# Optimization experiments

Measured on AMD Instinct MI355X. Metric: run time of the kernel, lower is better.

## Reference

```python
import jax, jax.numpy as jnp
import numpy as np

N, B, D_IN, HID = 1024, 8, 256, 256
L, SH, LH, GH = 2, 2, 4, 2
H = SH + LH + GH
DH = HID // H
EPS = 1e-5


def _sinusoidal_pe(n, d):
    pos = np.arange(n, dtype=np.float32)[:, None]
    i = np.arange(d, dtype=np.float32)[None, :]
    angle = pos / np.power(10000.0, (2.0 * np.floor(i / 2.0)) / d)
    pe = np.where((np.arange(d) % 2) == 0, np.sin(angle), np.cos(angle))
    return jnp.asarray(pe, jnp.float32)  # (n, d)


def _ln(x, g, b):
    mu = x.mean(-1, keepdims=True)
    var = ((x - mu) ** 2).mean(-1, keepdims=True)
    return (x - mu) * jax.lax.rsqrt(var + EPS) * g + b


def setup_inputs() -> dict:
    key = jax.random.key(0)
    ks = jax.random.split(key, 16)
    s = 0.02
    inp = {
        "nodes": jax.random.normal(ks[0], (N, B, D_IN), jnp.float32),
        "dist": jax.random.randint(ks[1], (B, N, N), 0, 6, jnp.int32),
        "W_in": jax.random.normal(ks[2], (D_IN, HID), jnp.float32) * s,
        "b_in": jnp.zeros((HID,), jnp.float32),
        "ln_in_g": jnp.ones((HID,), jnp.float32),
        "ln_in_b": jnp.zeros((HID,), jnp.float32),
        "Wqkv": jax.random.normal(ks[3], (L, HID, 3 * HID), jnp.float32) * s,
        "bqkv": jnp.zeros((L, 3 * HID), jnp.float32),
        "Wo": jax.random.normal(ks[4], (L, HID, HID), jnp.float32) * s,
        "bo": jnp.zeros((L, HID), jnp.float32),
        "ln1_g": jnp.ones((L, HID), jnp.float32),
        "ln1_b": jnp.zeros((L, HID), jnp.float32),
        "W1": jax.random.normal(ks[5], (L, HID, 2 * HID), jnp.float32) * s,
        "b1": jnp.zeros((L, 2 * HID), jnp.float32),
        "W2": jax.random.normal(ks[6], (L, 2 * HID, HID), jnp.float32) * s,
        "b2": jnp.zeros((L, HID), jnp.float32),
        "ln2_g": jnp.ones((L, HID), jnp.float32),
        "ln2_b": jnp.zeros((L, HID), jnp.float32),
        "bn_g": jnp.ones((HID,), jnp.float32),
        "bn_b": jnp.zeros((HID,), jnp.float32),
    }
    return inp


def reference(nodes, dist, W_in, b_in, ln_in_g, ln_in_b, Wqkv, bqkv, Wo, bo,
              ln1_g, ln1_b, W1, b1, W2, b2, ln2_g, ln2_b, bn_g, bn_b):
    # positional embedding (sinusoidal, added) + dense + LayerNorm; dropout=eval (identity)
    x = nodes + _sinusoidal_pe(N, D_IN)[:, None, :]          # (N,B,D_IN)
    x = _ln(x @ W_in + b_in, ln_in_g, ln_in_b)               # (N,B,HID)

    # dist_to_mask: per-head-group allowed patterns; True in torch mask = disallowed
    short = (dist == 1)[:, None]                             # (B,1,N,N)
    longm = (dist >= 1)[:, None]
    allowed = jnp.concatenate([
        jnp.broadcast_to(short, (B, SH, N, N)),
        jnp.broadcast_to(longm, (B, LH, N, N)),
        jnp.ones((B, GH, N, N), bool),
    ], axis=1)                                               # (B,H,N,N)
    bias = jnp.where(allowed, 0.0, -jnp.inf).astype(x.dtype)

    scale = 1.0 / np.sqrt(DH)
    for l in range(L):
        qkv = x @ Wqkv[l] + bqkv[l]                          # (N,B,3*HID)
        q, k, v = jnp.split(qkv, 3, axis=-1)
        def heads(t):  # (N,B,HID) -> (B,H,N,DH)
            return t.reshape(N, B, H, DH).transpose(1, 2, 0, 3)
        q, k, v = heads(q), heads(k), heads(v)
        s = jnp.einsum('bhnd,bhmd->bhnm', q, k) * scale + bias
        a = jax.nn.softmax(s, axis=-1)
        o = jnp.einsum('bhnm,bhmd->bhnd', a, v)              # (B,H,N,DH)
        o = o.transpose(2, 0, 1, 3).reshape(N, B, HID)
        x = _ln(x + o @ Wo[l] + bo[l], ln1_g[l], ln1_b[l])   # post-norm
        f = jax.nn.relu(x @ W1[l] + b1[l]) @ W2[l] + b2[l]
        x = _ln(x + f, ln2_g[l], ln2_b[l])

    y = x[0]                                                 # (B,HID) first position
    mu = y.mean(0)
    var = ((y - mu) ** 2).mean(0)
    return (y - mu) * jax.lax.rsqrt(var + EPS) * bn_g + bn_b
```

## Files before the change

### kernel.cpp

```cpp
#include <hip/hip_runtime.h>
#include <math.h>

constexpr int Nn = 1024, Bb = 8, HIDc = 256, Hh = 8, DHc = 32;
constexpr int TSTR = 520;

typedef __bf16 bf16x8 __attribute__((ext_vector_type(8)));
typedef __bf16 bf16x4 __attribute__((ext_vector_type(4)));
typedef float  f32x4  __attribute__((ext_vector_type(4)));

struct WCvtArgs {
    const float* src[9];
    int K[9], M[9], dstOff[9], tiles[9];
};

__global__ __launch_bounds__(256)
void prep_k(WCvtArgs a, __bf16* __restrict__ Wt,
            const int* __restrict__ dist, unsigned char* __restrict__ mp,
            const float* __restrict__ nodes, __bf16* __restrict__ xinb)
{
    __shared__ float ts[32][33];
    const int tid = threadIdx.x;
    if (blockIdx.x < 1088) {
        int bid = blockIdx.x, i = 0;
        while (bid >= a.tiles[i]) { bid -= a.tiles[i]; ++i; }
        const int K = a.K[i], M = a.M[i];
        const int tilesM = M >> 5;
        const int m0 = (bid % tilesM) << 5, k0 = (bid / tilesM) << 5;
        const float* src = a.src[i];
        __bf16* dst = Wt + a.dstOff[i];
        const int tx = tid & 31, ty = tid >> 5;
        #pragma unroll
        for (int j = 0; j < 4; ++j)
            ts[ty + 8 * j][tx] = src[(size_t)(k0 + ty + 8 * j) * M + m0 + tx];
        __syncthreads();
        #pragma unroll
        for (int j = 0; j < 4; ++j)
            dst[(size_t)(m0 + ty + 8 * j) * K + k0 + tx] = (__bf16)ts[tx][ty + 8 * j];
    } else if (blockIdx.x < 3136) {
        const int idx = (blockIdx.x - 1088) * 256 + tid;
        const int quad = idx & 3, c = (idx >> 2) & 15, q = (idx >> 6) & 1023, b = idx >> 16;
        const int* dp = dist + ((((size_t)b << 10) + q) << 10) + c * 64 + quad * 4;
        uchar4 out;
        unsigned char* po = &out.x;
        #pragma unroll
        for (int t = 0; t < 4; ++t) {
            const int4 v = *(const int4*)(dp + t * 16);
            unsigned int code = 0;
            const int dd[4] = {v.x, v.y, v.z, v.w};
            #pragma unroll
            for (int r = 0; r < 4; ++r)
                code |= ((dd[r] == 1 ? 1u : 0u) | (dd[r] >= 1 ? 2u : 0u)) << (2 * r);
            po[t] = (unsigned char)code;
        }
        *(uchar4*)(mp + ((((size_t)b << 10) + q) << 8) + (c << 4) + (quad << 2)) = out;
    } else {
        const int idx = (blockIdx.x - 3136) * 256 + tid;
        const int token = idx >> 7, k2 = (idx & 127) * 2;
        const int b = token >> 10, n = token & 1023;
        const float e = (float)k2 * (1.0f / 256.0f);
        const float freq = exp2f(-13.287712379549449f * e);
        const float ang = (float)n * freq;
        const float2 nd = *(const float2*)(nodes + ((size_t)(n * 8 + b)) * 256 + k2);
        __bf16* p = xinb + (size_t)token * 256 + k2;
        p[0] = (__bf16)(nd.x + sinf(ang));
        p[1] = (__bf16)(nd.y + cosf(ang));
    }
}

template<int KK, int NJ>
__device__ __forceinline__ void gemmT(const __bf16* __restrict__ wrow,
                                      const __bf16* __restrict__ x0,
                                      const __bf16* __restrict__ x1,
                                      f32x4 acc[4][2])
{
    constexpr int NKC = KK / 32;
    bf16x8 wA[4][4];
    #pragma unroll
    for (int p = 0; p < 4; ++p)
        #pragma unroll
        for (int t = 0; t < 4; ++t)
            wA[p][t] = *(const bf16x8*)(wrow + (size_t)(t * 16) * KK + p * 32);
    #pragma unroll
    for (int t = 0; t < 4; ++t) {
        acc[t][0] = (f32x4){0.f, 0.f, 0.f, 0.f};
        if (NJ == 2) acc[t][1] = (f32x4){0.f, 0.f, 0.f, 0.f};
    }
    #pragma unroll
    for (int kc = 0; kc < NKC; ++kc) {
        const bf16x8 b0 = *(const bf16x8*)(x0 + kc * 32);
        bf16x8 b1;
        if (NJ == 2) b1 = *(const bf16x8*)(x1 + kc * 32);
        const int cur = kc & 3;
        #pragma unroll
        for (int t = 0; t < 4; ++t) {
            acc[t][0] = __builtin_amdgcn_mfma_f32_16x16x32_bf16(wA[cur][t], b0, acc[t][0], 0, 0, 0);
            if (NJ == 2)
                acc[t][1] = __builtin_amdgcn_mfma_f32_16x16x32_bf16(wA[cur][t], b1, acc[t][1], 0, 0, 0);
        }
        if (kc + 4 < NKC)
            #pragma unroll
            for (int t = 0; t < 4; ++t)
                wA[cur][t] = *(const bf16x8*)(wrow + (size_t)(t * 16) * KK + (kc + 4) * 32);
    }
}

template<bool RESID, bool FFN, bool QKV, bool N0ROWS, bool XGATE, bool BNOUT, int NJ>
__global__ __launch_bounds__(256)
void layer_k(const __bf16* __restrict__ Ain, const float* __restrict__ xres,
             const __bf16* __restrict__ w0, const float* __restrict__ b0,
             const float* __restrict__ g1, const float* __restrict__ be1,
             const __bf16* __restrict__ w1, const float* __restrict__ b1_,
             const __bf16* __restrict__ w2, const float* __restrict__ b2_,
             const float* __restrict__ g2, const float* __restrict__ be2,
             const __bf16* __restrict__ wq, const float* __restrict__ bq, int qfull,
             const float* __restrict__ bng, const float* __restrict__ bnb,
             float* __restrict__ xout,
             __bf16* __restrict__ qb, __bf16* __restrict__ kb, __bf16* __restrict__ vtb)
{
    __shared__ __bf16 trans[32][TSTR];
    __shared__ float red[4][32][2];

    const int tid = threadIdx.x;
    const int lane = tid & 63;
    const int cq = tid >> 6;
    const int col = lane & 15, quad = lane >> 4;
    const int row0 = blockIdx.x * (NJ * 16);
    const int mb = cq * 64;

    #pragma unroll
    for (int i = 0; i < 2; ++i) {
        const int v = i * 256 + tid;
        const int rw = v >> 4, cc = (v & 15) * 16;
        const int rg = N0ROWS ? ((rw & 7) << 10) : (row0 + rw);
        *(bf16x8*)&trans[rw][cc]     = *(const bf16x8*)(Ain + (size_t)rg * 256 + cc);
        *(bf16x8*)&trans[rw][cc + 8] = *(const bf16x8*)(Ain + (size_t)rg * 256 + cc + 8);
    }
    __syncthreads();

    const __bf16* x0 = &trans[col][quad * 8];
    const __bf16* x1 = &trans[16 + col][quad * 8];
    int tg[2];
    #pragma unroll
    for (int j = 0; j < NJ; ++j)
        tg[j] = N0ROWS ? ((j * 16 + col) & 7) << 10 : (row0 + j * 16 + col);

    f32x4 acc[4][2];
    gemmT<256, NJ>(w0 + (size_t)(mb + col) * 256 + quad * 8, x0, x1, acc);

    float val[2][4][4];
    {
        float4 bb4[4], gm4[4], bt4[4];
        #pragma unroll
        for (int t = 0; t < 4; ++t) {
            const int cb = mb + t * 16 + quad * 4;
            bb4[t] = *(const float4*)&b0[cb];
            gm4[t] = *(const float4*)&g1[cb];
            bt4[t] = *(const float4*)&be1[cb];
        }
        #pragma unroll
        for (int j = 0; j < NJ; ++j) {
            float s1 = 0.f, s2 = 0.f;
            #pragma unroll
            for (int t = 0; t < 4; ++t) {
                float4 xr4 = {0.f, 0.f, 0.f, 0.f};
                if (RESID) xr4 = *(const float4*)&xres[(size_t)tg[j] * 256 + mb + t * 16 + quad * 4];
                const float* bbp = (const float*)&bb4[t];
                const float* xrp = (const float*)&xr4;
                #pragma unroll
                for (int r = 0; r < 4; ++r) {
                    float v = acc[t][j][r] + bbp[r] + xrp[r];
                    val[j][t][r] = v; s1 += v; s2 += v * v;
                }
            }
            s1 += __shfl_xor(s1, 16); s1 += __shfl_xor(s1, 32);
            s2 += __shfl_xor(s2, 16); s2 += __shfl_xor(s2, 32);
            if (quad == 0) { red[cq][j * 16 + col][0] = s1; red[cq][j * 16 + col][1] = s2; }
        }
        __syncthreads();
        #pragma unroll
        for (int j = 0; j < NJ; ++j) {
            const int tk = j * 16 + col;
            const float s1 = red[0][tk][0] + red[1][tk][0] + red[2][tk][0] + red[3][tk][0];
            const float s2 = red[0][tk][1] + red[1][tk][1] + red[2][tk][1] + red[3][tk][1];
            const float mu = s1 * (1.0f / 256.0f);
            const float rv = rsqrtf(s2 * (1.0f / 256.0f) - mu * mu + 1e-5f);
            #pragma unroll
            for (int t = 0; t < 4; ++t) {
                const float* gmp = (const float*)&gm4[t];
                const float* btp = (const float*)&bt4[t];
                bf16x4 o4; float4 of;
                #pragma unroll
                for (int r = 0; r < 4; ++r) {
                    const float o = (val[j][t][r] - mu) * rv * gmp[r] + btp[r];
                    val[j][t][r] = o;
                    o4[r] = (__bf16)o;
                    ((float*)&of)[r] = o;
                }
                *(bf16x4*)&trans[tk][mb + t * 16 + quad * 4] = o4;
                if (!FFN)
                    *(float4*)&xout[(size_t)tg[j] * 256 + mb + t * 16 + quad * 4] = of;
            }
        }
        __syncthreads();
    }

    if (FFN) {
        bf16x4 h1p[2][2][4];
        #pragma unroll
        for (int mh = 0; mh < 2; ++mh) {
            f32x4 a1[4][2];
            gemmT<256, NJ>(w1 + (size_t)(mh * 256 + mb + col) * 256 + quad * 8, x0, x1, a1);
            #pragma unroll
            for (int t = 0; t < 4; ++t) {
                const float4 bh4 = *(const float4*)&b1_[mh * 256 + mb + t * 16 + quad * 4];
                const float* bhp = (const float*)&bh4;
                #pragma unroll
                for (int j = 0; j < NJ; ++j)
                    #pragma unroll
                    for (int r = 0; r < 4; ++r)
                        h1p[mh][j][t][r] = (__bf16)fmaxf(a1[t][j][r] + bhp[r], 0.f);
            }
        }
        __syncthreads();
        #pragma unroll
        for (int mh = 0; mh < 2; ++mh)
            #pragma unroll
            for (int j = 0; j < NJ; ++j)
                #pragma unroll
                for (int t = 0; t < 4; ++t)
                    *(bf16x4*)&trans[j * 16 + col][mh * 256 + mb + t * 16 + quad * 4] = h1p[mh][j][t];
        __syncthreads();

        f32x4 a2[4][2];
        gemmT<512, NJ>(w2 + (size_t)(mb + col) * 512 + quad * 8, x0, x1, a2);

        float4 bb4[4], gm4[4], bt4[4];
        #pragma unroll
        for (int t = 0; t < 4; ++t) {
            const int cb = mb + t * 16 + quad * 4;
            bb4[t] = *(const float4*)&b2_[cb];
            gm4[t] = *(const float4*)&g2[cb];
            bt4[t] = *(const float4*)&be2[cb];
        }
        #pragma unroll
        for (int j = 0; j < NJ; ++j) {
            float s1 = 0.f, s2 = 0.f;
            #pragma unroll
            for (int t = 0; t < 4; ++t) {
                const float* bbp = (const float*)&bb4[t];
                #pragma unroll
                for (int r = 0; r < 4; ++r) {
                    const float v = a2[t][j][r] + bbp[r] + val[j][t][r];
                    val[j][t][r] = v; s1 += v; s2 += v * v;
                }
            }
            s1 += __shfl_xor(s1, 16); s1 += __shfl_xor(s1, 32);
            s2 += __shfl_xor(s2, 16); s2 += __shfl_xor(s2, 32);
            if (quad == 0) { red[cq][j * 16 + col][0] = s1; red[cq][j * 16 + col][1] = s2; }
        }
        __syncthreads();
        #pragma unroll
        for (int j = 0; j < NJ; ++j) {
            const int tk = j * 16 + col;
            const float s1 = red[0][tk][0] + red[1][tk][0] + red[2][tk][0] + red[3][tk][0];
            const float s2 = red[0][tk][1] + red[1][tk][1] + red[2][tk][1] + red[3][tk][1];
            const float mu = s1 * (1.0f / 256.0f);
            const float rv = rsqrtf(s2 * (1.0f / 256.0f) - mu * mu + 1e-5f);
            #pragma unroll
            for (int t = 0; t < 4; ++t) {
                const float* gmp = (const float*)&gm4[t];
                const float* btp = (const float*)&bt4[t];
                bf16x4 o4; float4 of;
                #pragma unroll
                for (int r = 0; r < 4; ++r) {
                    const float o = (val[j][t][r] - mu) * rv * gmp[r] + btp[r];
                    val[j][t][r] = o;
                    o4[r] = (__bf16)o;
                    ((float*)&of)[r] = o;
                }
                if (QKV) *(bf16x4*)&trans[tk][mb + t * 16 + quad * 4] = o4;
                if (!BNOUT) {
                    const bool wr = XGATE ? ((tg[j] & 1023) == 0) : true;
                    if (wr) *(float4*)&xout[(size_t)tg[j] * 256 + mb + t * 16 + quad * 4] = of;
                }
            }
        }
        if (BNOUT) {
            #pragma unroll
            for (int t = 0; t < 4; ++t) {
                const int cb = mb + t * 16 + quad * 4;
                const float4 g4 = *(const float4*)&bng[cb];
                const float4 bB = *(const float4*)&bnb[cb];
                float4 of;
                #pragma unroll
                for (int r = 0; r < 4; ++r) {
                    float s1 = val[0][t][r], s2 = val[0][t][r] * val[0][t][r];
                    s1 += __shfl_xor(s1, 1); s2 += __shfl_xor(s2, 1);
                    s1 += __shfl_xor(s1, 2); s2 += __shfl_xor(s2, 2);
                    s1 += __shfl_xor(s1, 4); s2 += __shfl_xor(s2, 4);
                    s1 += __shfl_xor(s1, 8); s2 += __shfl_xor(s2, 8);
                    const float mu = s1 * (1.0f / 16.0f);
                    const float rv = rsqrtf(s2 * (1.0f / 16.0f) - mu * mu + 1e-5f);
                    ((float*)&of)[r] = (val[0][t][r] - mu) * rv * ((const float*)&g4)[r]
                                       + ((const float*)&bB)[r];
                }
                if (col < 8)
                    *(float4*)&xout[(size_t)col * 256 + cb] = of;
            }
        }
        __syncthreads();
    }

    if (QKV) {
        const int b_ = N0ROWS ? 0 : (row0 >> 10);
        const bool qneed = qfull || ((row0 & 1023) < 128);
        for (int cg = 0; cg < 3; ++cg) {
            if (cg == 0 && !qneed) continue;
            f32x4 aq[4][2];
            gemmT<256, NJ>(wq + (size_t)(cg * 256 + mb + col) * 256 + quad * 8, x0, x1, aq);
            const float qs = (cg == 0) ? 0.25505402616305625f : 1.0f;
            #pragma unroll
            for (int t = 0; t < 4; ++t) {
                const int cc = mb + t * 16;
                const int h = cc >> 5;
                const int dhb = (cc & 31) + quad * 4;
                const float4 bq4 = *(const float4*)&bq[cg * 256 + cc + quad * 4];
                const float* bqp = (const float*)&bq4;
                #pragma unroll
                for (int j = 0; j < NJ; ++j) {
                    const int n = tg[j] & 1023;
                    if (cg == 2) {
                        #pragma unroll
                        for (int r = 0; r < 4; ++r)
                            vtb[((size_t)(b_ * 8 + h) * 32 + dhb + r) * 1024 + n] =
                                (__bf16)(aq[t][j][r] + bqp[r]);
                    } else {
                        bf16x4 p;
                        #pragma unroll
                        for (int r = 0; r < 4; ++r)
                            p[r] = (__bf16)((aq[t][j][r] + bqp[r]) * qs);
                        __bf16* dst = (cg == 0) ? qb : kb;
                        *(bf16x4*)&dst[((size_t)(b_ * 8 + h) * 1024 + n) * 32 + dhb] = p;
                    }
                }
            }
        }
    }
}

__global__ __launch_bounds__(256)
void attn_mfma(const __bf16* __restrict__ Qb, const __bf16* __restrict__ Kb,
               const __bf16* __restrict__ Vt, const unsigned char* __restrict__ MP,
               __bf16* __restrict__ O)
{
    __shared__ __bf16 pbuf[2][4][2][16][72];
    const int tid = threadIdx.x;
    const int lane = tid & 63;
    const int wv = tid >> 6;
    const int col = lane & 15;
    const int quad = lane >> 4;
    const int xr = blockIdx.x;
    const int bh = ((xr & 7) << 3) | (xr >> 3);
    const int b = bh >> 3, h = bh & 7;
    const int qbase = blockIdx.y * 128 + wv * 32;
    const int hsel = (h < 2) ? 0 : 1;
    const bool masked = (h < 6);

    bf16x8 qf[2];
    #pragma unroll
    for (int j = 0; j < 2; ++j)
        qf[j] = *(const bf16x8*)(Qb + ((size_t)bh * Nn + qbase + j * 16 + col) * DHc + quad * 8);

    bf16x8 onesf;
    {
        const __bf16 one = (__bf16)1.0f, zero = (__bf16)0.0f;
        #pragma unroll
        for (int j = 0; j < 8; ++j) onesf[j] = (col == 0) ? one : zero;
    }

    f32x4 O0[2], O1[2], OL[2];
    #pragma unroll
    for (int j = 0; j < 2; ++j) {
        O0[j] = (f32x4){0.f, 0.f, 0.f, 0.f};
        O1[j] = (f32x4){0.f, 0.f, 0.f, 0.f};
        OL[j] = (f32x4){0.f, 0.f, 0.f, 0.f};
    }
    const f32x4 zf = {0.f, 0.f, 0.f, 0.f};
    const __bf16* kbase = Kb + (size_t)bh * Nn * DHc;

    bf16x8 kf[4];
    #pragma unroll
    for (int t = 0; t < 4; ++t)
        kf[t] = *(const bf16x8*)(kbase + (size_t)(t * 16 + col) * DHc + quad * 8);

    for (int c = 0; c < 16; ++c) {
        bf16x8 kn[4];
        if (c < 15)
            #pragma unroll
            for (int t = 0; t < 4; ++t)
                kn[t] = *(const bf16x8*)(kbase + (size_t)((c + 1) * 64 + t * 16 + col) * DHc + quad * 8);
        uchar4 mk[2];
        if (masked)
            #pragma unroll
            for (int j = 0; j < 2; ++j)
                mk[j] = *(const uchar4*)(MP + ((((size_t)b << 10) + qbase + j * 16 + col) << 8)
                                            + (c << 4) + (quad << 2));
        #pragma unroll
        for (int j = 0; j < 2; ++j) {
            f32x4 S[4];
            #pragma unroll
            for (int t = 0; t < 4; ++t)
                S[t] = __builtin_amdgcn_mfma_f32_16x16x32_bf16(kf[t], qf[j], zf, 0, 0, 0);
            if (masked) {
                const unsigned char mb2[4] = {mk[j].x, mk[j].y, mk[j].z, mk[j].w};
                #pragma unroll
                for (int t = 0; t < 4; ++t)
                    #pragma unroll
                    for (int r = 0; r < 4; ++r)
                        if (!((mb2[t] >> (2 * r + hsel)) & 1)) S[t][r] = -INFINITY;
            }
            #pragma unroll
            for (int t = 0; t < 4; ++t) {
                bf16x4 p4;
                #pragma unroll
                for (int r = 0; r < 4; ++r)
                    p4[r] = (__bf16)__builtin_amdgcn_exp2f(S[t][r]);
                *(bf16x4*)(&pbuf[c & 1][wv][j][col][t * 16 + quad * 4]) = p4;
            }
        }
        const __bf16* vp = Vt + (size_t)bh * DHc * Nn + c * 64 + quad * 8;
        #pragma unroll
        for (int kh = 0; kh < 2; ++kh) {
            const bf16x8 v0 = *(const bf16x8*)(vp + (size_t)col * Nn + kh * 32);
            const bf16x8 v1 = *(const bf16x8*)(vp + (size_t)(col + 16) * Nn + kh * 32);
            #pragma unroll
            for (int j = 0; j < 2; ++j) {
                const bf16x8 pf = *(const bf16x8*)(&pbuf[c & 1][wv][j][col][kh * 32 + quad * 8]);
                O0[j] = __builtin_amdgcn_mfma_f32_16x16x32_bf16(pf, v0, O0[j], 0, 0, 0);
                O1[j] = __builtin_amdgcn_mfma_f32_16x16x32_bf16(pf, v1, O1[j], 0, 0, 0);
                OL[j] = __builtin_amdgcn_mfma_f32_16x16x32_bf16(pf, onesf, OL[j], 0, 0, 0);
            }
        }
        if (c < 15)
            #pragma unroll
            for (int t = 0; t < 4; ++t) kf[t] = kn[t];
    }
    #pragma unroll
    for (int j = 0; j < 2; ++j)
        #pragma unroll
        for (int r = 0; r < 4; ++r) {
            const float Lr = __shfl(OL[j][r], lane & 48);
            const float inv = 1.0f / Lr;
            const int q = qbase + j * 16 + quad * 4 + r;
            __bf16* op = O + ((size_t)(b * 1024 + q)) * 256 + h * 32 + col;
            op[0]  = (__bf16)(O0[j][r] * inv);
            op[16] = (__bf16)(O1[j][r] * inv);
        }
}

extern "C" void kernel_launch(void* const* d_in, const int* in_sizes, int n_in,
                              void* d_out, int out_size, void* d_ws, size_t ws_size,
                              hipStream_t stream)
{
    const float* nodes   = (const float*)d_in[0];
    const int*   dist    = (const int*)  d_in[1];
    const float* W_in    = (const float*)d_in[2];
    const float* b_in    = (const float*)d_in[3];
    const float* ln_in_g = (const float*)d_in[4];
    const float* ln_in_b = (const float*)d_in[5];
    const float* Wqkv    = (const float*)d_in[6];
    const float* bqkv    = (const float*)d_in[7];
    const float* Wo      = (const float*)d_in[8];
    const float* bo      = (const float*)d_in[9];
    const float* ln1_g   = (const float*)d_in[10];
    const float* ln1_b   = (const float*)d_in[11];
    const float* W1      = (const float*)d_in[12];
    const float* b1      = (const float*)d_in[13];
    const float* W2      = (const float*)d_in[14];
    const float* b2      = (const float*)d_in[15];
    const float* ln2_g   = (const float*)d_in[16];
    const float* ln2_b   = (const float*)d_in[17];
    const float* bn_g    = (const float*)d_in[18];
    const float* bn_b    = (const float*)d_in[19];

    char* ws = (char*)d_ws;
    float*  x   = (float*)(ws);
    unsigned char* mp = (unsigned char*)(ws + 8388608);
    __bf16* wt  = (__bf16*)(ws + 10485760);
    __bf16* qb  = (__bf16*)(ws + 12845056);
    __bf16* kb  = (__bf16*)(ws + 17039360);
    __bf16* vtb = (__bf16*)(ws + 21233664);
    __bf16* ob  = (__bf16*)(ws + 25427968);
    __bf16* xinb = ob;

    WCvtArgs wa;
    wa.src[0] = W_in;           wa.K[0] = 256; wa.M[0] = 256; wa.dstOff[0] = 0;
    wa.src[1] = Wqkv;           wa.K[1] = 256; wa.M[1] = 768; wa.dstOff[1] = 65536;
    wa.src[2] = Wqkv + 196608;  wa.K[2] = 256; wa.M[2] = 768; wa.dstOff[2] = 262144;
    wa.src[3] = Wo;             wa.K[3] = 256; wa.M[3] = 256; wa.dstOff[3] = 458752;
    wa.src[4] = Wo + 65536;     wa.K[4] = 256; wa.M[4] = 256; wa.dstOff[4] = 524288;
    wa.src[5] = W1;             wa.K[5] = 256; wa.M[5] = 512; wa.dstOff[5] = 589824;
    wa.src[6] = W1 + 131072;    wa.K[6] = 256; wa.M[6] = 512; wa.dstOff[6] = 720896;
    wa.src[7] = W2;             wa.K[7] = 512; wa.M[7] = 256; wa.dstOff[7] = 851968;
    wa.src[8] = W2 + 131072;    wa.K[8] = 512; wa.M[8] = 256; wa.dstOff[8] = 983040;
    for (int i = 0; i < 9; ++i) wa.tiles[i] = (wa.K[i] >> 5) * (wa.M[i] >> 5);

    prep_k<<<7232, 256, 0, stream>>>(wa, wt, dist, mp, nodes, xinb);

    layer_k<false, false, true, false, false, false, 2><<<256, 256, 0, stream>>>(
        xinb, nullptr, wt, b_in, ln_in_g, ln_in_b,
        nullptr, nullptr, nullptr, nullptr, nullptr, nullptr,
        wt + 65536, bqkv, 1, nullptr, nullptr, x, qb, kb, vtb);

    attn_mfma<<<dim3(64, 8), 256, 0, stream>>>(qb, kb, vtb, mp, ob);

    layer_k<true, true, true, false, true, false, 2><<<256, 256, 0, stream>>>(
        ob, x, wt + 458752, bo, ln1_g, ln1_b,
        wt + 589824, b1, wt + 851968, b2, ln2_g, ln2_b,
        wt + 262144, bqkv + 768, 0, nullptr, nullptr, x, qb, kb, vtb);

    attn_mfma<<<dim3(64, 1), 256, 0, stream>>>(qb, kb, vtb, mp, ob);

    layer_k<true, true, false, true, true, true, 1><<<1, 256, 0, stream>>>(
        ob, x, wt + 524288, bo + 256, ln1_g + 256, ln1_b + 256,
        wt + 720896, b1 + 512, wt + 983040, b2 + 256, ln2_g + 256, ln2_b + 256,
        nullptr, nullptr, 0, bn_g, bn_b, (float*)d_out, nullptr, nullptr, nullptr);
}
```

Baseline: 267.3 us.

## Split layer kernel output columns across 8 waves instead of 4

The fused layer kernel now launches 512 threads per block, with each of 8 waves computing 32 output columns (one head) instead of 64. The GEMM helper is rewritten to hold 2 column tiles with 8-deep K-chunk weight prefetch, and the LayerNorm reductions sum over 8 wave partials. This is meant to double wave-level parallelism and hide weight-load latency in the latency-bound per-row-block GEMMs. In exchange it adds more barrier participants and a larger reduction buffer, and each wave reuses its activation operands over fewer tiles.

```diff
diff --git a/kernel.cpp b/kernel.cpp
--- a/kernel.cpp
+++ b/kernel.cpp
@@ -68,44 +68,69 @@
 }
 
 template<int KK, int NJ>
-__device__ __forceinline__ void gemmT(const __bf16* __restrict__ wrow,
+__device__ __forceinline__ void gemmW(const __bf16* __restrict__ wrow,
                                       const __bf16* __restrict__ x0,
                                       const __bf16* __restrict__ x1,
-                                      f32x4 acc[4][2])
+                                      f32x4 acc[2][2])
 {
     constexpr int NKC = KK / 32;
-    bf16x8 wA[4][4];
-    #pragma unroll
-    for (int p = 0; p < 4; ++p)
-        #pragma unroll
-        for (int t = 0; t < 4; ++t)
-            wA[p][t] = *(const bf16x8*)(wrow + (size_t)(t * 16) * KK + p * 32);
-    #pragma unroll
-    for (int t = 0; t < 4; ++t) {
+    bf16x8 wA[2][8];
+    #pragma unroll
+    for (int kc = 0; kc < (NKC > 8 ? 8 : NKC); ++kc)
+        #pragma unroll
+        for (int t = 0; t < 2; ++t)
+            wA[t][kc] = *(const bf16x8*)(wrow + (size_t)(t * 16) * KK + kc * 32);
+    #pragma unroll
+    for (int t = 0; t < 2; ++t) {
         acc[t][0] = (f32x4){0.f, 0.f, 0.f, 0.f};
         if (NJ == 2) acc[t][1] = (f32x4){0.f, 0.f, 0.f, 0.f};
     }
-    #pragma unroll
-    for (int kc = 0; kc < NKC; ++kc) {
-        const bf16x8 b0 = *(const bf16x8*)(x0 + kc * 32);
-        bf16x8 b1;
-        if (NJ == 2) b1 = *(const bf16x8*)(x1 + kc * 32);
-        const int cur = kc & 3;
-        #pragma unroll
-        for (int t = 0; t < 4; ++t) {
-            acc[t][0] = __builtin_amdgcn_mfma_f32_16x16x32_bf16(wA[cur][t], b0, acc[t][0], 0, 0, 0);
-            if (NJ == 2)
-                acc[t][1] = __builtin_amdgcn_mfma_f32_16x16x32_bf16(wA[cur][t], b1, acc[t][1], 0, 0, 0);
-        }
-        if (kc + 4 < NKC)
-            #pragma unroll
-            for (int t = 0; t < 4; ++t)
-                wA[cur][t] = *(const bf16x8*)(wrow + (size_t)(t * 16) * KK + (kc + 4) * 32);
+    if constexpr (NKC <= 8) {
+        #pragma unroll
+        for (int kc = 0; kc < NKC; ++kc) {
+            const bf16x8 b0 = *(const bf16x8*)(x0 + kc * 32);
+            bf16x8 b1;
+            if (NJ == 2) b1 = *(const bf16x8*)(x1 + kc * 32);
+            #pragma unroll
+            for (int t = 0; t < 2; ++t) {
+                acc[t][0] = __builtin_amdgcn_mfma_f32_16x16x32_bf16(wA[t][kc], b0, acc[t][0], 0, 0, 0);
+                if (NJ == 2)
+                    acc[t][1] = __builtin_amdgcn_mfma_f32_16x16x32_bf16(wA[t][kc], b1, acc[t][1], 0, 0, 0);
+            }
+        }
+    } else {
+        #pragma unroll
+        for (int kc = 0; kc < 8; ++kc) {
+            const bf16x8 b0 = *(const bf16x8*)(x0 + kc * 32);
+            bf16x8 b1;
+            if (NJ == 2) b1 = *(const bf16x8*)(x1 + kc * 32);
+            #pragma unroll
+            for (int t = 0; t < 2; ++t) {
+                acc[t][0] = __builtin_amdgcn_mfma_f32_16x16x32_bf16(wA[t][kc], b0, acc[t][0], 0, 0, 0);
+                if (NJ == 2)
+                    acc[t][1] = __builtin_amdgcn_mfma_f32_16x16x32_bf16(wA[t][kc], b1, acc[t][1], 0, 0, 0);
+            }
+            #pragma unroll
+            for (int t = 0; t < 2; ++t)
+                wA[t][kc] = *(const bf16x8*)(wrow + (size_t)(t * 16) * KK + (kc + 8) * 32);
+        }
+        #pragma unroll
+        for (int kc = 8; kc < 16; ++kc) {
+            const bf16x8 b0 = *(const bf16x8*)(x0 + kc * 32);
+            bf16x8 b1;
+            if (NJ == 2) b1 = *(const bf16x8*)(x1 + kc * 32);
+            #pragma unroll
+            for (int t = 0; t < 2; ++t) {
+                acc[t][0] = __builtin_amdgcn_mfma_f32_16x16x32_bf16(wA[t][kc - 8], b0, acc[t][0], 0, 0, 0);
+                if (NJ == 2)
+                    acc[t][1] = __builtin_amdgcn_mfma_f32_16x16x32_bf16(wA[t][kc - 8], b1, acc[t][1], 0, 0, 0);
+            }
+        }
     }
 }
 
 template<bool RESID, bool FFN, bool QKV, bool N0ROWS, bool XGATE, bool BNOUT, int NJ>
-__global__ __launch_bounds__(256)
+__global__ __launch_bounds__(512)
 void layer_k(const __bf16* __restrict__ Ain, const float* __restrict__ xres,
              const __bf16* __restrict__ w0, const float* __restrict__ b0,
              const float* __restrict__ g1, const float* __restrict__ be1,
@@ -118,22 +143,21 @@
              __bf16* __restrict__ qb, __bf16* __restrict__ kb, __bf16* __restrict__ vtb)
 {
     __shared__ __bf16 trans[32][TSTR];
-    __shared__ float red[4][32][2];
+    __shared__ float red[8][32][2];
 
     const int tid = threadIdx.x;
     const int lane = tid & 63;
-    const int cq = tid >> 6;
+    const int wv = tid >> 6;
     const int col = lane & 15, quad = lane >> 4;
     const int row0 = blockIdx.x * (NJ * 16);
-    const int mb = cq * 64;
-
-    #pragma unroll
-    for (int i = 0; i < 2; ++i) {
-        const int v = i * 256 + tid;
-        const int rw = v >> 4, cc = (v & 15) * 16;
+    const int ms = wv * 32;
+
+    #pragma unroll
+    for (int i = 0; i < NJ; ++i) {
+        const int v = i * 512 + tid;
+        const int rw = v >> 5, cc = (v & 31) * 8;
         const int rg = N0ROWS ? ((rw & 7) << 10) : (row0 + rw);
-        *(bf16x8*)&trans[rw][cc]     = *(const bf16x8*)(Ain + (size_t)rg * 256 + cc);
-        *(bf16x8*)&trans[rw][cc + 8] = *(const bf16x8*)(Ain + (size_t)rg * 256 + cc + 8);
+        *(bf16x8*)&trans[rw][cc] = *(const bf16x8*)(Ain + (size_t)rg * 256 + cc);
     }
     __syncthreads();
 
@@ -144,15 +168,15 @@
     for (int j = 0; j < NJ; ++j)
         tg[j] = N0ROWS ? ((j * 16 + col) & 7) << 10 : (row0 + j * 16 + col);
 
-    f32x4 acc[4][2];
-    gemmT<256, NJ>(w0 + (size_t)(mb + col) * 256 + quad * 8, x0, x1, acc);
-
-    float val[2][4][4];
+    f32x4 acc[2][2];
+    gemmW<256, NJ>(w0 + (size_t)(ms + col) * 256 + quad * 8, x0, x1, acc);
+
+    float val[2][2][4];
     {
-        float4 bb4[4], gm4[4], bt4[4];
-        #pragma unroll
-        for (int t = 0; t < 4; ++t) {
-            const int cb = mb + t * 16 + quad * 4;
+        float4 bb4[2], gm4[2], bt4[2];
+        #pragma unroll
+        for (int t = 0; t < 2; ++t) {
+            const int cb = ms + t * 16 + quad * 4;
             bb4[t] = *(const float4*)&b0[cb];
             gm4[t] = *(const float4*)&g1[cb];
             bt4[t] = *(const float4*)&be1[cb];
@@ -161,9 +185,9 @@
         for (int j = 0; j < NJ; ++j) {
             float s1 = 0.f, s2 = 0.f;
             #pragma unroll
-            for (int t = 0; t < 4; ++t) {
+            for (int t = 0; t < 2; ++t) {
                 float4 xr4 = {0.f, 0.f, 0.f, 0.f};
-                if (RESID) xr4 = *(const float4*)&xres[(size_t)tg[j] * 256 + mb + t * 16 + quad * 4];
+                if (RESID) xr4 = *(const float4*)&xres[(size_t)tg[j] * 256 + ms + t * 16 + quad * 4];
                 const float* bbp = (const float*)&bb4[t];
                 const float* xrp = (const float*)&xr4;
                 #pragma unroll
@@ -174,18 +198,19 @@
             }
             s1 += __shfl_xor(s1, 16); s1 += __shfl_xor(s1, 32);
             s2 += __shfl_xor(s2, 16); s2 += __shfl_xor(s2, 32);
-            if (quad == 0) { red[cq][j * 16 + col][0] = s1; red[cq][j * 16 + col][1] = s2; }
+            if (quad == 0) { red[wv][j * 16 + col][0] = s1; red[wv][j * 16 + col][1] = s2; }
         }
         __syncthreads();
         #pragma unroll
         for (int j = 0; j < NJ; ++j) {
             const int tk = j * 16 + col;
-            const float s1 = red[0][tk][0] + red[1][tk][0] + red[2][tk][0] + red[3][tk][0];
-            const float s2 = red[0][tk][1] + red[1][tk][1] + red[2][tk][1] + red[3][tk][1];
+            float s1 = 0.f, s2 = 0.f;
+            #pragma unroll
+            for (int w = 0; w < 8; ++w) { s1 += red[w][tk][0]; s2 += red[w][tk][1]; }
             const float mu = s1 * (1.0f / 256.0f);
             const float rv = rsqrtf(s2 * (1.0f / 256.0f) - mu * mu + 1e-5f);
             #pragma unroll
-            for (int t = 0; t < 4; ++t) {
+            for (int t = 0; t < 2; ++t) {
                 const float* gmp = (const float*)&gm4[t];
                 const float* btp = (const float*)&bt4[t];
                 bf16x4 o4; float4 of;
@@ -196,23 +221,23 @@
                     o4[r] = (__bf16)o;
                     ((float*)&of)[r] = o;
                 }
-                *(bf16x4*)&trans[tk][mb + t * 16 + quad * 4] = o4;
+                *(bf16x4*)&trans[tk][ms + t * 16 + quad * 4] = o4;
                 if (!FFN)
-                    *(float4*)&xout[(size_t)tg[j] * 256 + mb + t * 16 + quad * 4] = of;
+                    *(float4*)&xout[(size_t)tg[j] * 256 + ms + t * 16 + quad * 4] = of;
             }
         }
         __syncthreads();
     }
 
     if (FFN) {
-        bf16x4 h1p[2][2][4];
+        bf16x4 h1p[2][2][2];
         #pragma unroll
         for (int mh = 0; mh < 2; ++mh) {
-            f32x4 a1[4][2];
-            gemmT<256, NJ>(w1 + (size_t)(mh * 256 + mb + col) * 256 + quad * 8, x0, x1, a1);
-            #pragma unroll
-            for (int t = 0; t < 4; ++t) {
-                const float4 bh4 = *(const float4*)&b1_[mh * 256 + mb + t * 16 + quad * 4];
+            f32x4 a1[2][2];
+            gemmW<256, NJ>(w1 + (size_t)(mh * 256 + ms + col) * 256 + quad * 8, x0, x1, a1);
+            #pragma unroll
+            for (int t = 0; t < 2; ++t) {
+                const float4 bh4 = *(const float4*)&b1_[mh * 256 + ms + t * 16 + quad * 4];
                 const float* bhp = (const float*)&bh4;
                 #pragma unroll
                 for (int j = 0; j < NJ; ++j)
@@ -227,17 +252,17 @@
             #pragma unroll
             for (int j = 0; j < NJ; ++j)
                 #pragma unroll
-                for (int t = 0; t < 4; ++t)
-                    *(bf16x4*)&trans[j * 16 + col][mh * 256 + mb + t * 16 + quad * 4] = h1p[mh][j][t];
-        __syncthreads();
-
-        f32x4 a2[4][2];
-        gemmT<512, NJ>(w2 + (size_t)(mb + col) * 512 + quad * 8, x0, x1, a2);
-
-        float4 bb4[4], gm4[4], bt4[4];
-        #pragma unroll
-        for (int t = 0; t < 4; ++t) {
-            const int cb = mb + t * 16 + quad * 4;
+                for (int t = 0; t < 2; ++t)
+                    *(bf16x4*)&trans[j * 16 + col][mh * 256 + ms + t * 16 + quad * 4] = h1p[mh][j][t];
+        __syncthreads();
+
+        f32x4 a2[2][2];
+        gemmW<512, NJ>(w2 + (size_t)(ms + col) * 512 + quad * 8, x0, x1, a2);
+
+        float4 bb4[2], gm4[2], bt4[2];
+        #pragma unroll
+        for (int t = 0; t < 2; ++t) {
+            const int cb = ms + t * 16 + quad * 4;
             bb4[t] = *(const float4*)&b2_[cb];
             gm4[t] = *(const float4*)&g2[cb];
             bt4[t] = *(const float4*)&be2[cb];
@@ -246,7 +271,7 @@
         for (int j = 0; j < NJ; ++j) {
             float s1 = 0.f, s2 = 0.f;
             #pragma unroll
-            for (int t = 0; t < 4; ++t) {
+            for (int t = 0; t < 2; ++t) {
                 const float* bbp = (const float*)&bb4[t];
                 #pragma unroll
                 for (int r = 0; r < 4; ++r) {
@@ -256,18 +281,19 @@
             }
             s1 += __shfl_xor(s1, 16); s1 += __shfl_xor(s1, 32);
             s2 += __shfl_xor(s2, 16); s2 += __shfl_xor(s2, 32);
-            if (quad == 0) { red[cq][j * 16 + col][0] = s1; red[cq][j * 16 + col][1] = s2; }
+            if (quad == 0) { red[wv][j * 16 + col][0] = s1; red[wv][j * 16 + col][1] = s2; }
         }
         __syncthreads();
         #pragma unroll
         for (int j = 0; j < NJ; ++j) {
             const int tk = j * 16 + col;
-            const float s1 = red[0][tk][0] + red[1][tk][0] + red[2][tk][0] + red[3][tk][0];
-            const float s2 = red[0][tk][1] + red[1][tk][1] + red[2][tk][1] + red[3][tk][1];
+            float s1 = 0.f, s2 = 0.f;
+            #pragma unroll
+            for (int w = 0; w < 8; ++w) { s1 += red[w][tk][0]; s2 += red[w][tk][1]; }
             const float mu = s1 * (1.0f / 256.0f);
             const float rv = rsqrtf(s2 * (1.0f / 256.0f) - mu * mu + 1e-5f);
             #pragma unroll
-            for (int t = 0; t < 4; ++t) {
+            for (int t = 0; t < 2; ++t) {
                 const float* gmp = (const float*)&gm4[t];
                 const float* btp = (const float*)&bt4[t];
                 bf16x4 o4; float4 of;
@@ -278,17 +304,17 @@
                     o4[r] = (__bf16)o;
                     ((float*)&of)[r] = o;
                 }
-                if (QKV) *(bf16x4*)&trans[tk][mb + t * 16 + quad * 4] = o4;
+                if (QKV) *(bf16x4*)&trans[tk][ms + t * 16 + quad * 4] = o4;
                 if (!BNOUT) {
                     const bool wr = XGATE ? ((tg[j] & 1023) == 0) : true;
-                    if (wr) *(float4*)&xout[(size_t)tg[j] * 256 + mb + t * 16 + quad * 4] = of;
+                    if (wr) *(float4*)&xout[(size_t)tg[j] * 256 + ms + t * 16 + quad * 4] = of;
                 }
             }
         }
         if (BNOUT) {
             #pragma unroll
-            for (int t = 0; t < 4; ++t) {
-                const int cb = mb + t * 16 + quad * 4;
+            for (int t = 0; t < 2; ++t) {
+                const int cb = ms + t * 16 + quad * 4;
                 const float4 g4 = *(const float4*)&bng[cb];
                 const float4 bB = *(const float4*)&bnb[cb];
                 float4 of;
@@ -314,17 +340,16 @@
     if (QKV) {
         const int b_ = N0ROWS ? 0 : (row0 >> 10);
         const bool qneed = qfull || ((row0 & 1023) < 128);
+        const int h = wv;
         for (int cg = 0; cg < 3; ++cg) {
             if (cg == 0 && !qneed) continue;
-            f32x4 aq[4][2];
-            gemmT<256, NJ>(wq + (size_t)(cg * 256 + mb + col) * 256 + quad * 8, x0, x1, aq);
+            f32x4 aq[2][2];
+            gemmW<256, NJ>(wq + (size_t)(cg * 256 + ms + col) * 256 + quad * 8, x0, x1, aq);
             const float qs = (cg == 0) ? 0.25505402616305625f : 1.0f;
             #pragma unroll
-            for (int t = 0; t < 4; ++t) {
-                const int cc = mb + t * 16;
-                const int h = cc >> 5;
-                const int dhb = (cc & 31) + quad * 4;
-                const float4 bq4 = *(const float4*)&bq[cg * 256 + cc + quad * 4];
+            for (int t = 0; t < 2; ++t) {
+                const int dhb = t * 16 + quad * 4;
+                const float4 bq4 = *(const float4*)&bq[cg * 256 + ms + dhb];
                 const float* bqp = (const float*)&bq4;
                 #pragma unroll
                 for (int j = 0; j < NJ; ++j) {
@@ -507,21 +532,21 @@
 
     prep_k<<<7232, 256, 0, stream>>>(wa, wt, dist, mp, nodes, xinb);
 
-    layer_k<false, false, true, false, false, false, 2><<<256, 256, 0, stream>>>(
+    layer_k<false, false, true, false, false, false, 2><<<256, 512, 0, stream>>>(
         xinb, nullptr, wt, b_in, ln_in_g, ln_in_b,
         nullptr, nullptr, nullptr, nullptr, nullptr, nullptr,
         wt + 65536, bqkv, 1, nullptr, nullptr, x, qb, kb, vtb);
 
     attn_mfma<<<dim3(64, 8), 256, 0, stream>>>(qb, kb, vtb, mp, ob);
 
-    layer_k<true, true, true, false, true, false, 2><<<256, 256, 0, stream>>>(
+    layer_k<true, true, true, false, true, false, 2><<<256, 512, 0, stream>>>(
         ob, x, wt + 458752, bo, ln1_g, ln1_b,
         wt + 589824, b1, wt + 851968, b2, ln2_g, ln2_b,
         wt + 262144, bqkv + 768, 0, nullptr, nullptr, x, qb, kb, vtb);
 
     attn_mfma<<<dim3(64, 1), 256, 0, stream>>>(qb, kb, vtb, mp, ob);
 
-    layer_k<true, true, false, true, true, true, 1><<<1, 256, 0, stream>>>(
+    layer_k<true, true, false, true, true, true, 1><<<1, 512, 0, stream>>>(
         ob, x, wt + 524288, bo + 256, ln1_g + 256, ln1_b + 256,
         wt + 720896, b1 + 512, wt + 983040, b2 + 256, ln2_g + 256, ln2_b + 256,
         nullptr, nullptr, 0, bn_g, bn_b, (float*)d_out, nullptr, nullptr, nullptr);
```

After: 258.7 us. 3.2% less time.
